# Kernel optimization log

Measured on AMD Instinct MI355X. Metric: run time of the kernel, lower is better.

## Reference

```python
import jax, jax.numpy as jnp
from jax import lax
import numpy as np

B = 64          # batch
HW = 28         # image height/width (hardcoded in module)
LATENT = 256    # latent_size
LABEL = 10      # label_size
FEAT = 64 * HW * HW  # 50176, encoder/decoder fc feature dim


def _conv(x, w, pad):
    # x: [N,C,H,W], w: [O,I,kH,kW]
    return lax.conv_general_dilated(
        x, w, (1, 1), ((pad, pad), (pad, pad)),
        dimension_numbers=('NCHW', 'OIHW', 'NCHW'))


def _conv_transpose(x, w, b, pad):
    # ConvTranspose2d(stride=1, padding=pad) == conv with flipped, transposed
    # kernel and padding k-1-pad. w: [I,O,kH,kW] (torch ConvTranspose layout).
    k = w.shape[2]
    wt = jnp.flip(w, (2, 3)).transpose(1, 0, 2, 3)  # [O,I,kH,kW]
    return _conv(x, wt, k - 1 - pad) + b[None, :, None, None]


def _encoder(images, c1w, c1b, c2w, c2b, fcw, fcb):
    x = jax.nn.relu(_conv(images, c1w, 2) + c1b[None, :, None, None])
    x = jax.nn.relu(_conv(x, c2w, 2) + c2b[None, :, None, None])
    x = x.reshape(x.shape[0], FEAT)
    return jnp.tanh(x @ fcw.T + fcb)


def _decoder(z, fcw, fcb, ct2w, ct2b, ct1w, ct1b):
    x = jnp.arctanh(z)
    x = (x @ fcw.T + fcb).reshape(-1, 64, HW, HW)
    x = jax.nn.relu(_conv_transpose(x, ct2w, ct2b, 2))
    return _conv_transpose(x, ct1w, ct1b, 2)


def _hopfield_weight(patterns):
    # TrainHopfield: Hebbian outer-product sum with mean subtraction,
    # zero diagonal, normalized by number of patterns. One GEMM.
    rho = jnp.mean(patterns)
    t = patterns - rho                      # [L, latent]
    w = t.T @ t                             # [latent, latent]
    w = w - jnp.diag(jnp.diag(w))
    return w / patterns.shape[0]


def _cluster(s0, w):
    # Batched version of: iterate s = sign(w @ s) up to LATENT steps,
    # stopping per-sample when energy -s@w@s stops changing.
    def energy(s):
        return -jnp.einsum('bi,ij,bj->b', s, w, s)

    def step(carry, _):
        s, prev_e, done = carry
        new_s = jnp.sign(s @ w.T)           # w symmetric; per-sample w@s
        e = energy(new_s)
        s_next = jnp.where(done[:, None], s, new_s)
        prev_e_next = jnp.where(done, prev_e, e)
        done_next = done | (e == prev_e)
        return (s_next, prev_e_next, done_next), None

    init = (s0, energy(s0), jnp.zeros(s0.shape[0], dtype=bool))
    (s, _, _), _ = lax.scan(step, init, None, length=LATENT)
    return s


def setup_inputs() -> dict:
    key = jax.random.key(0)
    ks = jax.random.split(key, 12)
    s = 0.05
    f32 = jnp.float32
    return {
        'images': jax.random.normal(ks[0], (B, 1, HW, HW), f32),
        'enc_c1_w': jax.random.normal(ks[1], (32, 1, 5, 5), f32) * s,
        'enc_c1_b': jnp.zeros((32,), f32),
        'enc_c2_w': jax.random.normal(ks[2], (64, 32, 5, 5), f32) * s,
        'enc_c2_b': jnp.zeros((64,), f32),
        'enc_fc_w': jax.random.normal(ks[3], (LATENT, FEAT), f32) * 0.005,
        'enc_fc_b': jnp.zeros((LATENT,), f32),
        'dec_fc_w': jax.random.normal(ks[4], (FEAT, LATENT), f32) * s,
        'dec_fc_b': jnp.zeros((FEAT,), f32),
        'dec_ct2_w': jax.random.normal(ks[5], (64, 32, 5, 5), f32) * s,
        'dec_ct2_b': jnp.zeros((32,), f32),
        'dec_ct1_w': jax.random.normal(ks[6], (32, 1, 5, 5), f32) * s,
        'dec_ct1_b': jnp.zeros((1,), f32),
        'sm_w': jax.random.normal(ks[7], (LABEL, LATENT), f32) * s,
        'sm_b': jnp.zeros((LABEL,), f32),
        'label_latent': jnp.tanh(jax.random.normal(ks[8], (LABEL, LATENT), f32)),
    }


def reference(images, enc_c1_w, enc_c1_b, enc_c2_w, enc_c2_b, enc_fc_w,
              enc_fc_b, dec_fc_w, dec_fc_b, dec_ct2_w, dec_ct2_b, dec_ct1_w,
              dec_ct1_b, sm_w, sm_b, label_latent):
    z = _encoder(images, enc_c1_w, enc_c1_b, enc_c2_w, enc_c2_b,
                 enc_fc_w, enc_fc_b)                       # [B, latent]
    w = _hopfield_weight(jnp.sign(label_latent))           # [latent, latent]
    s0 = lax.stop_gradient(jnp.sign(z))                    # detached copy
    clustered = _cluster(s0, w)                            # [B, latent]
    cluster_probs = jax.nn.softmax(clustered @ label_latent.T, axis=1)
    class_probs = jax.nn.softmax(z @ sm_w.T + sm_b, axis=1)
    recon = _decoder(z, dec_fc_w, dec_fc_b, dec_ct2_w, dec_ct2_b,
                     dec_ct1_w, dec_ct1_b)                 # [B,1,28,28]
    return (cluster_probs, class_probs, recon)
```

## Files before the change

kernel.cpp:

```cpp
#include <hip/hip_runtime.h>
#include <hip/hip_bf16.h>
#include <math.h>

#define BATCH 64
#define HW 28
#define PIX 784
#define LATENT 256
#define LABEL 10
#define FEAT 50176
#define KS 7
#define KCH 7168
#define TSTR 36

typedef __attribute__((ext_vector_type(8))) short bf16x8;
typedef __attribute__((ext_vector_type(4))) float f32x4;

__device__ __forceinline__ float sgnf(float v) {
    return (v > 0.f) ? 1.f : ((v < 0.f) ? -1.f : 0.f);
}

__device__ __forceinline__ short f2bf(float f) {
    union { float f; unsigned u; } v; v.f = f;
    unsigned r = v.u + 0x7FFF + ((v.u >> 16) & 1);
    return (short)(r >> 16);
}
__device__ __forceinline__ float bf2f(short s) {
    union { unsigned u; float f; } v; v.u = ((unsigned)(unsigned short)s) << 16;
    return v.f;
}

template<int G, int FLIP>
__global__ __launch_bounds__(256) void conv5_k(const float* __restrict__ in,
                        const float* __restrict__ w,
                        const float* __restrict__ bias, float* __restrict__ out,
                        int IC, int OC, int relu) {
    int b = blockIdx.x, oc0 = blockIdx.y * G;
    __shared__ float plp[2][32 * TSTR];
    int tid = threadIdx.x;

    for (int t = tid; t < 2 * 32 * TSTR; t += 256) ((float*)plp)[t] = 0.f;

    bool actS = tid < 196;
    int ys = tid / 7, qs = tid % 7;

    int q = tid & 7, yy = tid >> 3;
    bool actC = (q < 7) && (yy < 28);
    int x0 = q * 4;

    float acc[G][4];
    #pragma unroll
    for (int g = 0; g < G; ++g)
        #pragma unroll
        for (int xi = 0; xi < 4; ++xi) acc[g][xi] = 0.f;

    __syncthreads();
    if (actS) {
        float4 v = *(const float4*)&in[((size_t)(b * IC + 0)) * PIX + tid * 4];
        *(float2*)&plp[0][(ys + 2) * TSTR + 4 * qs + 2] = make_float2(v.x, v.y);
        *(float2*)&plp[0][(ys + 2) * TSTR + 4 * qs + 4] = make_float2(v.z, v.w);
    }
    __syncthreads();

    for (int ic = 0; ic < IC; ++ic) {
        float4 vn;
        bool more = (ic + 1) < IC;
        if (more && actS)
            vn = *(const float4*)&in[((size_t)(b * IC + ic + 1)) * PIX + tid * 4];

        const float* tile = plp[ic & 1];
        if (actC) {
            #pragma unroll
            for (int dy = 0; dy < 5; ++dy) {
                float4 ra = *(const float4*)&tile[(yy + dy) * TSTR + x0];
                float4 rb = *(const float4*)&tile[(yy + dy) * TSTR + x0 + 4];
                float rw[8] = {ra.x, ra.y, ra.z, ra.w, rb.x, rb.y, rb.z, rb.w};
                #pragma unroll
                for (int g = 0; g < G; ++g) {
                    #pragma unroll
                    for (int dx = 0; dx < 5; ++dx) {
                        float wv = FLIP
                            ? w[((size_t)ic * OC + (oc0 + g)) * 25 + (4 - dy) * 5 + (4 - dx)]
                            : w[((size_t)(oc0 + g) * IC + ic) * 25 + dy * 5 + dx];
                        #pragma unroll
                        for (int xi = 0; xi < 4; ++xi)
                            acc[g][xi] += rw[xi + dx] * wv;
                    }
                }
            }
        }
        if (more && actS) {
            float* nt = plp[(ic + 1) & 1];
            *(float2*)&nt[(ys + 2) * TSTR + 4 * qs + 2] = make_float2(vn.x, vn.y);
            *(float2*)&nt[(ys + 2) * TSTR + 4 * qs + 4] = make_float2(vn.z, vn.w);
        }
        __syncthreads();
    }

    if (actC) {
        #pragma unroll
        for (int g = 0; g < G; ++g) {
            float bv = bias[oc0 + g];
            float4 o;
            o.x = acc[g][0] + bv;
            o.y = acc[g][1] + bv;
            o.z = acc[g][2] + bv;
            o.w = acc[g][3] + bv;
            if (relu) {
                o.x = fmaxf(o.x, 0.f); o.y = fmaxf(o.y, 0.f);
                o.z = fmaxf(o.z, 0.f); o.w = fmaxf(o.w, 0.f);
            }
            *(float4*)&out[((size_t)(b * OC + (oc0 + g))) * PIX + yy * HW + x0] = o;
        }
    }
}

__global__ __launch_bounds__(64) void c2_mfma_k(const short* __restrict__ xh,
                        const short* __restrict__ xm, const short* __restrict__ xl,
                        const short* __restrict__ wb,
                        const float* __restrict__ bias, float* __restrict__ out) {
    int b = blockIdx.x;
    int t0 = blockIdx.y * 4;
    int lane = threadIdx.x;
    int prow = lane & 15, kgrp = lane >> 4;

    f32x4 acc[4][4];
    #pragma unroll
    for (int pt = 0; pt < 4; ++pt)
        #pragma unroll
        for (int nt = 0; nt < 4; ++nt) acc[pt][nt] = (f32x4){0.f, 0.f, 0.f, 0.f};

    int py[4], px[4];
    bool ptv[4];
    #pragma unroll
    for (int pt = 0; pt < 4; ++pt) {
        int p = (t0 + pt) * 16 + prow;
        ptv[pt] = (t0 + pt) < 49;
        py[pt] = p / 28; px[pt] = p % 28;
    }

    for (int tap = 0; tap < 25; ++tap) {
        int dy = tap / 5 - 2, dx = tap % 5 - 2;
        const short* wt = wb + (size_t)tap * 2048;
        bf16x8 B0[4], B1[4], B2[4];
        #pragma unroll
        for (int nt = 0; nt < 4; ++nt) {
            int off = (nt * 16 + prow) * 32 + kgrp * 8;
            B0[nt] = *(const bf16x8*)&wt[off];
            B1[nt] = *(const bf16x8*)&wt[51200 + off];
            B2[nt] = *(const bf16x8*)&wt[102400 + off];
        }
        #pragma unroll
        for (int pt = 0; pt < 4; ++pt) {
            int ysrc = py[pt] + dy, xsrc = px[pt] + dx;
            bool valid = ptv[pt] && (ysrc >= 0) && (ysrc < 28) && (xsrc >= 0) && (xsrc < 28);
            bf16x8 ah = {0,0,0,0,0,0,0,0}, am = {0,0,0,0,0,0,0,0}, al = {0,0,0,0,0,0,0,0};
            if (valid) {
                size_t o = ((size_t)b * PIX + ysrc * 28 + xsrc) * 32 + kgrp * 8;
                ah = *(const bf16x8*)&xh[o];
                am = *(const bf16x8*)&xm[o];
                al = *(const bf16x8*)&xl[o];
            }
            #pragma unroll
            for (int nt = 0; nt < 4; ++nt) {
                acc[pt][nt] = __builtin_amdgcn_mfma_f32_16x16x32_bf16(ah, B0[nt], acc[pt][nt], 0, 0, 0);
                acc[pt][nt] = __builtin_amdgcn_mfma_f32_16x16x32_bf16(ah, B1[nt], acc[pt][nt], 0, 0, 0);
                acc[pt][nt] = __builtin_amdgcn_mfma_f32_16x16x32_bf16(am, B0[nt], acc[pt][nt], 0, 0, 0);
                acc[pt][nt] = __builtin_amdgcn_mfma_f32_16x16x32_bf16(ah, B2[nt], acc[pt][nt], 0, 0, 0);
                acc[pt][nt] = __builtin_amdgcn_mfma_f32_16x16x32_bf16(am, B1[nt], acc[pt][nt], 0, 0, 0);
                acc[pt][nt] = __builtin_amdgcn_mfma_f32_16x16x32_bf16(al, B0[nt], acc[pt][nt], 0, 0, 0);
            }
        }
    }

    __shared__ float ot[64][17];
    float bv = bias[lane];
    for (int pt = 0; pt < 4; ++pt) {
        if (!ptv[pt]) continue;
        #pragma unroll
        for (int nt = 0; nt < 4; ++nt)
            #pragma unroll
            for (int r = 0; r < 4; ++r)
                ot[nt * 16 + prow][kgrp * 4 + r] = acc[pt][nt][r];
        float* op = &out[((size_t)(b * 64 + lane)) * PIX + (t0 + pt) * 16];
        #pragma unroll
        for (int i = 0; i < 4; ++i) {
            float4 o;
            o.x = fmaxf(ot[lane][i * 4 + 0] + bv, 0.f);
            o.y = fmaxf(ot[lane][i * 4 + 1] + bv, 0.f);
            o.z = fmaxf(ot[lane][i * 4 + 2] + bv, 0.f);
            o.w = fmaxf(ot[lane][i * 4 + 3] + bv, 0.f);
            *(float4*)&op[i * 4] = o;
        }
    }
}

__global__ void xsplit3_k(const float* __restrict__ x, short* __restrict__ xh,
                          short* __restrict__ xm, short* __restrict__ xl) {
    __shared__ float lds[32][17];
    int b = blockIdx.x, pbase = blockIdx.y * 16;
    int t = threadIdx.x;
    if (t < 128) {
        int ic = t >> 2, pj = (t & 3) * 4;
        float4 v = *(const float4*)&x[((size_t)(b * 32 + ic)) * PIX + pbase + pj];
        lds[ic][pj + 0] = v.x; lds[ic][pj + 1] = v.y;
        lds[ic][pj + 2] = v.z; lds[ic][pj + 3] = v.w;
    }
    __syncthreads();
    int p = t >> 4, ic2 = (t & 15) * 2;
    size_t o = ((size_t)b * PIX + pbase + p) * 32 + ic2;
    short2 h, m, l;
    {
        float v = lds[ic2][p];
        short s0 = f2bf(v); float r = v - bf2f(s0);
        short s1 = f2bf(r); float r2 = r - bf2f(s1);
        h.x = s0; m.x = s1; l.x = f2bf(r2);
    }
    {
        float v = lds[ic2 + 1][p];
        short s0 = f2bf(v); float r = v - bf2f(s0);
        short s1 = f2bf(r); float r2 = r - bf2f(s1);
        h.y = s0; m.y = s1; l.y = f2bf(r2);
    }
    *(short2*)&xh[o] = h;
    *(short2*)&xm[o] = m;
    *(short2*)&xl[o] = l;
}

__global__ void wprep3_k(const float* __restrict__ w, short* __restrict__ wb) {
    int j = blockIdx.x * 256 + threadIdx.x;
    if (j < 51200) {
        int ic = j & 31;
        int oc = (j >> 5) & 63;
        int tap = j >> 11;
        float v = w[((size_t)oc * 32 + ic) * 25 + tap];
        short s0 = f2bf(v); float r = v - bf2f(s0);
        short s1 = f2bf(r); float r2 = r - bf2f(s1);
        wb[j] = s0;
        wb[51200 + j] = s1;
        wb[102400 + j] = f2bf(r2);
    }
}

__global__ __launch_bounds__(64) void ct2_mfma_k(const short* __restrict__ xb,
                        const short* __restrict__ wb,
                        const float* __restrict__ bias, float* __restrict__ out) {
    int b = blockIdx.x;
    int pbase = blockIdx.y * 16;
    int lane = threadIdx.x;
    int prow = lane & 15;
    int kgrp = lane >> 4;
    int p = pbase + prow;
    int py = p / 28, px = p % 28;

    f32x4 acc0 = {0.f, 0.f, 0.f, 0.f};
    f32x4 acc1 = {0.f, 0.f, 0.f, 0.f};

    for (int tap = 0; tap < 25; ++tap) {
        int dy = tap / 5 - 2, dx = tap % 5 - 2;
        int ysrc = py + dy, xsrc = px + dx;
        bool valid = (ysrc >= 0) && (ysrc < 28) && (xsrc >= 0) && (xsrc < 28);
        int ps = ysrc * 28 + xsrc;

        bf16x8 a0 = {0,0,0,0,0,0,0,0}, a1 = {0,0,0,0,0,0,0,0};
        if (valid) {
            const bf16x8* ap = (const bf16x8*)&xb[((size_t)b * PIX + ps) * 64 + kgrp * 8];
            a0 = ap[0];
            a1 = ap[4];
        }
        const short* wt = &wb[(size_t)tap * 32 * 64];
        int oc_l = lane & 15;
        bf16x8 b00 = *(const bf16x8*)&wt[oc_l * 64 + kgrp * 8];
        bf16x8 b01 = *(const bf16x8*)&wt[oc_l * 64 + 32 + kgrp * 8];
        bf16x8 b10 = *(const bf16x8*)&wt[(16 + oc_l) * 64 + kgrp * 8];
        bf16x8 b11 = *(const bf16x8*)&wt[(16 + oc_l) * 64 + 32 + kgrp * 8];

        acc0 = __builtin_amdgcn_mfma_f32_16x16x32_bf16(a0, b00, acc0, 0, 0, 0);
        acc0 = __builtin_amdgcn_mfma_f32_16x16x32_bf16(a1, b01, acc0, 0, 0, 0);
        acc1 = __builtin_amdgcn_mfma_f32_16x16x32_bf16(a0, b10, acc1, 0, 0, 0);
        acc1 = __builtin_amdgcn_mfma_f32_16x16x32_bf16(a1, b11, acc1, 0, 0, 0);
    }

    __shared__ float ot[32][16];
    int drow = (lane >> 4) * 4;
    #pragma unroll
    for (int r = 0; r < 4; ++r) {
        ot[lane & 15][drow + r]        = acc0[r];
        ot[16 + (lane & 15)][drow + r] = acc1[r];
    }
    __syncthreads();
    int oc = lane >> 1, ph = (lane & 1) * 8;
    float bv = bias[oc];
    float4 o0, o1;
    o0.x = fmaxf(ot[oc][ph + 0] + bv, 0.f);
    o0.y = fmaxf(ot[oc][ph + 1] + bv, 0.f);
    o0.z = fmaxf(ot[oc][ph + 2] + bv, 0.f);
    o0.w = fmaxf(ot[oc][ph + 3] + bv, 0.f);
    o1.x = fmaxf(ot[oc][ph + 4] + bv, 0.f);
    o1.y = fmaxf(ot[oc][ph + 5] + bv, 0.f);
    o1.z = fmaxf(ot[oc][ph + 6] + bv, 0.f);
    o1.w = fmaxf(ot[oc][ph + 7] + bv, 0.f);
    float* op = &out[((size_t)(b * 32 + oc)) * PIX + pbase + ph];
    *(float4*)&op[0] = o0;
    *(float4*)&op[4] = o1;
}

__global__ void wprep_k(const float* __restrict__ w, short* __restrict__ wb) {
    int j = blockIdx.x * 256 + threadIdx.x;
    if (j < 25 * 32 * 64) {
        int ic = j & 63;
        int oc = (j >> 6) & 31;
        int tap = j >> 11;
        int dyi = tap / 5, dxi = tap % 5;
        wb[j] = f2bf(w[((size_t)ic * 32 + oc) * 25 + (4 - dyi) * 5 + (4 - dxi)]);
    }
}

__global__ void xpose_k(const float* __restrict__ x, short* __restrict__ xb) {
    __shared__ short lds[64][16];
    int b = blockIdx.x, pbase = blockIdx.y * 16;
    int t = threadIdx.x;
    {
        int ic = t >> 2, pj = (t & 3) * 4;
        float4 v = *(const float4*)&x[((size_t)(b * 64 + ic)) * PIX + pbase + pj];
        lds[ic][pj + 0] = f2bf(v.x);
        lds[ic][pj + 1] = f2bf(v.y);
        lds[ic][pj + 2] = f2bf(v.z);
        lds[ic][pj + 3] = f2bf(v.w);
    }
    __syncthreads();
    {
        int p = t >> 4, icq = (t & 15) * 4;
        short4 s;
        s.x = lds[icq + 0][p];
        s.y = lds[icq + 1][p];
        s.z = lds[icq + 2][p];
        s.w = lds[icq + 3][p];
        *(short4*)&xb[((size_t)b * PIX + pbase + p) * 64 + icq] = s;
    }
}

__global__ void enc_fc_part_k(const float* __restrict__ x, const float* __restrict__ w,
                              float* __restrict__ part) {
    int n0 = blockIdx.x * 4;
    int ks = blockIdx.y;
    int kl = threadIdx.x & 31;
    int mi = threadIdx.x >> 5;

    float acc[8][4];
    #pragma unroll
    for (int mg = 0; mg < 8; ++mg)
        #pragma unroll
        for (int nt = 0; nt < 4; ++nt) acc[mg][nt] = 0.f;

    int kend = (ks + 1) * KCH;
    for (int kk = ks * KCH + kl * 4; kk < kend; kk += 128) {
        float4 xv[8];
        #pragma unroll
        for (int mg = 0; mg < 8; ++mg)
            xv[mg] = *(const float4*)&x[(size_t)(mg * 8 + mi) * FEAT + kk];
        #pragma unroll
        for (int nt = 0; nt < 4; ++nt) {
            float4 wv = *(const float4*)&w[(size_t)(n0 + nt) * FEAT + kk];
            #pragma unroll
            for (int mg = 0; mg < 8; ++mg) {
                acc[mg][nt] += xv[mg].x * wv.x + xv[mg].y * wv.y
                             + xv[mg].z * wv.z + xv[mg].w * wv.w;
            }
        }
    }

    #pragma unroll
    for (int mg = 0; mg < 8; ++mg) {
        #pragma unroll
        for (int nt = 0; nt < 4; ++nt) {
            float v = acc[mg][nt];
            v += __shfl_xor(v, 16, 64);
            v += __shfl_xor(v, 8, 64);
            v += __shfl_xor(v, 4, 64);
            v += __shfl_xor(v, 2, 64);
            v += __shfl_xor(v, 1, 64);
            if (kl == 0)
                part[(ks * BATCH + (mg * 8 + mi)) * LATENT + (n0 + nt)] = v;
        }
    }
}

__global__ void enc_fc_fin_k(const float* __restrict__ part, const float* __restrict__ bias,
                             float* __restrict__ z, float* __restrict__ xsaT) {
    int m = blockIdx.x;
    int n = threadIdx.x;
    int idx = m * 256 + n;
    float a = bias[n];
    for (int ksi = 0; ksi < KS; ++ksi) a += part[ksi * BATCH * LATENT + idx];
    float zv = tanhf(a);
    z[idx] = zv;
    xsaT[n * BATCH + m] = atanhf(zv);
}

__global__ void hop_rho_k(const float* __restrict__ ll, float* __restrict__ rho_out) {
    float p = 0.f;
    for (int t = threadIdx.x; t < LABEL * LATENT; t += 256) p += sgnf(ll[t]);
    __shared__ float red[8];
    for (int o = 32; o; o >>= 1) p += __shfl_down(p, o, 64);
    if ((threadIdx.x & 63) == 0) red[threadIdx.x >> 6] = p;
    __syncthreads();
    if (threadIdx.x == 0)
        rho_out[0] = (red[0] + red[1] + red[2] + red[3]) / (float)(LABEL * LATENT);
}

__global__ void hop_w_k(const float* __restrict__ ll, const float* __restrict__ rho_p,
                        float* __restrict__ wout) {
    int i = blockIdx.x, j = threadIdx.x;
    float rho = rho_p[0];
    float acc = 0.f;
    #pragma unroll
    for (int l = 0; l < LABEL; ++l) {
        float a = sgnf(ll[l * LATENT + i]) - rho;
        float b = sgnf(ll[l * LATENT + j]) - rho;
        acc += a * b;
    }
    wout[i * LATENT + j] = (i == j) ? 0.f : acc / 10.f;
}

__global__ __launch_bounds__(1024) void cluster_k(const float* __restrict__ z,
                          const float* __restrict__ w,
                          const float* __restrict__ ll, float* __restrict__ out) {
    int b = blockIdx.x;
    int t = threadIdx.x;
    int i = t & 255;
    int q = t >> 8;
    int lane = t & 63;
    int wvid = t >> 6;

    __shared__ float s_sh[LATENT];
    __shared__ float part[1024];
    __shared__ float red[4];
    __shared__ float cflag[4];
    __shared__ int ctl_sh;
    __shared__ float logit[LABEL];

    float wreg[64];
    #pragma unroll
    for (int jj = 0; jj < 64; ++jj)
        wreg[jj] = w[(q * 64 + jj) * LATENT + i];

    float s_cur = 0.f, s_old = 2.f, v = 0.f;
    float e_prev = 0.f;
    if (q == 0) {
        s_cur = sgnf(z[b * LATENT + i]);
        s_sh[i] = s_cur;
    }
    __syncthreads();

    {
        float p0 = 0.f, p1 = 0.f;
        #pragma unroll
        for (int jj = 0; jj < 64; jj += 2) {
            p0 += wreg[jj]     * s_sh[q * 64 + jj];
            p1 += wreg[jj + 1] * s_sh[q * 64 + jj + 1];
        }
        part[t] = p0 + p1;
    }
    __syncthreads();
    if (q == 0) {
        v = part[i] + part[i + 256] + part[i + 512] + part[i + 768];
        float p = s_cur * v;
        #pragma unroll
        for (int o = 32; o; o >>= 1) p += __shfl_down(p, o, 64);
        if (lane == 0) red[wvid] = p;
    }
    __syncthreads();
    if (t == 0) e_prev = -(red[0] + red[1] + red[2] + red[3]);

    for (int it = 0; it < LATENT; ++it) {
        if (q == 0) {
            float ns = sgnf(v);
            unsigned long long m = __ballot(ns == s_old);
            if (lane == 0) cflag[wvid] = (m == ~0ull) ? 1.f : 0.f;
            s_sh[i] = ns;
            s_old = s_cur;
            s_cur = ns;
        }
        __syncthreads();
        {
            float p0 = 0.f, p1 = 0.f;
            #pragma unroll
            for (int jj = 0; jj < 64; jj += 2) {
                p0 += wreg[jj]     * s_sh[q * 64 + jj];
                p1 += wreg[jj + 1] * s_sh[q * 64 + jj + 1];
            }
            part[t] = p0 + p1;
        }
        __syncthreads();
        if (q == 0) {
            v = part[i] + part[i + 256] + part[i + 512] + part[i + 768];
            float p = s_cur * v;
            #pragma unroll
            for (int o = 32; o; o >>= 1) p += __shfl_down(p, o, 64);
            if (lane == 0) red[wvid] = p;
        }
        __syncthreads();
        if (t == 0) {
            float e = -(red[0] + red[1] + red[2] + red[3]);
            int c = 0;
            if (e == e_prev) c = 1;
            else if (it >= 1 && cflag[0] != 0.f && cflag[1] != 0.f &&
                     cflag[2] != 0.f && cflag[3] != 0.f)
                c = (((LATENT - 1 - it) & 1) == 0) ? 2 : 3;
            else e_prev = e;
            ctl_sh = c;
        }
        __syncthreads();
        int c = ctl_sh;
        if (c != 0) {
            if (c == 3 && q == 0) s_sh[i] = s_old;
            break;
        }
    }
    __syncthreads();

    if (wvid < LABEL) {
        float p = 0.f;
        #pragma unroll
        for (int r = 0; r < 4; ++r)
            p += s_sh[r * 64 + lane] * ll[wvid * LATENT + r * 64 + lane];
        #pragma unroll
        for (int o = 32; o; o >>= 1) p += __shfl_down(p, o, 64);
        if (lane == 0) logit[wvid] = p;
    }
    __syncthreads();
    if (t == 0) {
        float mx = logit[0];
        for (int c = 1; c < LABEL; ++c) mx = fmaxf(mx, logit[c]);
        float ex[LABEL];
        float s = 0.f;
        for (int c = 0; c < LABEL; ++c) { ex[c] = expf(logit[c] - mx); s += ex[c]; }
        for (int c = 0; c < LABEL; ++c) out[b * LABEL + c] = ex[c] / s;
    }
}

__device__ __forceinline__ float block_sum256(float p, float* red) {
    __syncthreads();
    for (int o = 32; o; o >>= 1) p += __shfl_down(p, o, 64);
    if ((threadIdx.x & 63) == 0) red[threadIdx.x >> 6] = p;
    __syncthreads();
    return red[0] + red[1] + red[2] + red[3];
}

__global__ void class_k(const float* __restrict__ z, const float* __restrict__ smw,
                        const float* __restrict__ smb, float* __restrict__ out) {
    int b = blockIdx.x;
    int i = threadIdx.x;
    __shared__ float red[8];
    __shared__ float logit[LABEL];
    float zi = z[b * LATENT + i];
    for (int c = 0; c < LABEL; ++c) {
        float p = zi * smw[c * LATENT + i];
        float t = block_sum256(p, red);
        if (i == 0) logit[c] = t + smb[c];
    }
    __syncthreads();
    if (i == 0) {
        float mx = logit[0];
        for (int c = 1; c < LABEL; ++c) mx = fmaxf(mx, logit[c]);
        float ex[LABEL];
        float s = 0.f;
        for (int c = 0; c < LABEL; ++c) { ex[c] = expf(logit[c] - mx); s += ex[c]; }
        for (int c = 0; c < LABEL; ++c) out[b * LABEL + c] = ex[c] / s;
    }
}

__global__ __launch_bounds__(256) void dec_fc_k(const float* __restrict__ xsa,
                         const float* __restrict__ w,
                         const float* __restrict__ bias, float* __restrict__ y) {
    __shared__ float xs[128 * BATCH];
    __shared__ float wt[64 * 128];
    int tid = threadIdx.x;
    int lane = tid & 63;
    int wv = tid >> 6;
    int n0 = blockIdx.x * 64;

    float acc[16];
    #pragma unroll
    for (int nt = 0; nt < 16; ++nt) acc[nt] = 0.f;

    float4 xr[8], wr[8];
    #pragma unroll
    for (int i = 0; i < 8; ++i) {
        int j = i * 1024 + tid * 4;
        xr[i] = *(const float4*)&xsa[j];
        int row = j >> 7, col = j & 127;
        wr[i] = *(const float4*)&w[(size_t)(n0 + row) * LATENT + col];
    }
    #pragma unroll
    for (int i = 0; i < 8; ++i) {
        int j = i * 1024 + tid * 4;
        *(float4*)&xs[j] = xr[i];
        *(float4*)&wt[j] = wr[i];
    }
    __syncthreads();

    #pragma unroll
    for (int i = 0; i < 8; ++i) {
        int j = i * 1024 + tid * 4;
        xr[i] = *(const float4*)&xsa[8192 + j];
        int row = j >> 7, col = j & 127;
        wr[i] = *(const float4*)&w[(size_t)(n0 + row) * LATENT + 128 + col];
    }

    for (int kq = 0; kq < 32; ++kq) {
        int k0 = kq * 4;
        float xv0 = xs[(k0 + 0) * BATCH + lane];
        float xv1 = xs[(k0 + 1) * BATCH + lane];
        float xv2 = xs[(k0 + 2) * BATCH + lane];
        float xv3 = xs[(k0 + 3) * BATCH + lane];
        #pragma unroll
        for (int nt = 0; nt < 16; ++nt) {
            float4 wv4 = *(const float4*)&wt[(wv * 16 + nt) * 128 + k0];
            acc[nt] += xv0 * wv4.x + xv1 * wv4.y + xv2 * wv4.z + xv3 * wv4.w;
        }
    }
    __syncthreads();

    #pragma unroll
    for (int i = 0; i < 8; ++i) {
        int j = i * 1024 + tid * 4;
        *(float4*)&xs[j] = xr[i];
        *(float4*)&wt[j] = wr[i];
    }
    __syncthreads();

    for (int kq = 0; kq < 32; ++kq) {
        int k0 = kq * 4;
        float xv0 = xs[(k0 + 0) * BATCH + lane];
        float xv1 = xs[(k0 + 1) * BATCH + lane];
        float xv2 = xs[(k0 + 2) * BATCH + lane];
        float xv3 = xs[(k0 + 3) * BATCH + lane];
        #pragma unroll
        for (int nt = 0; nt < 16; ++nt) {
            float4 wv4 = *(const float4*)&wt[(wv * 16 + nt) * 128 + k0];
            acc[nt] += xv0 * wv4.x + xv1 * wv4.y + xv2 * wv4.z + xv3 * wv4.w;
        }
    }

    int nbase = n0 + wv * 16;
    #pragma unroll
    for (int nq = 0; nq < 4; ++nq) {
        float4 o;
        o.x = acc[nq * 4 + 0] + bias[nbase + nq * 4 + 0];
        o.y = acc[nq * 4 + 1] + bias[nbase + nq * 4 + 1];
        o.z = acc[nq * 4 + 2] + bias[nbase + nq * 4 + 2];
        o.w = acc[nq * 4 + 3] + bias[nbase + nq * 4 + 3];
        *(float4*)&y[(size_t)lane * FEAT + nbase + nq * 4] = o;
    }
}

extern "C" void kernel_launch(void* const* d_in, const int* in_sizes, int n_in,
                              void* d_out, int out_size, void* d_ws, size_t ws_size,
                              hipStream_t stream) {
    const float* images   = (const float*)d_in[0];
    const float* c1w      = (const float*)d_in[1];
    const float* c1b      = (const float*)d_in[2];
    const float* c2w      = (const float*)d_in[3];
    const float* c2b      = (const float*)d_in[4];
    const float* efw      = (const float*)d_in[5];
    const float* efb      = (const float*)d_in[6];
    const float* dfw      = (const float*)d_in[7];
    const float* dfb      = (const float*)d_in[8];
    const float* ct2w     = (const float*)d_in[9];
    const float* ct2b     = (const float*)d_in[10];
    const float* ct1w     = (const float*)d_in[11];
    const float* ct1b     = (const float*)d_in[12];
    const float* smw      = (const float*)d_in[13];
    const float* smb      = (const float*)d_in[14];
    const float* ll       = (const float*)d_in[15];

    float* out = (float*)d_out;
    float* ws  = (float*)d_ws;

    float* big0 = ws;
    float* big1 = ws + 3211264;
    float* part = ws + 3211264 + 1605632;
    float* z    = part + KS * BATCH * LATENT;
    float* whop = z + BATCH * LATENT;
    float* rho  = whop + LATENT * LATENT;
    float* xsa  = rho + 4;
    short* xbf  = (short*)(xsa + 16384);
    short* wbf  = (short*)(xsa + 16384 + 1605632);
    short* xh3  = xbf;
    short* xm3  = xbf + 1605632;
    short* xl3  = (short*)(xsa + 16384 + 1605632 + 25600);
    short* wb3  = xl3 + 1605632;

    conv5_k<4,0><<<dim3(BATCH, 8), 256, 0, stream>>>(images, c1w, c1b, big1, 1, 32, 1);
    wprep3_k<<<200, 256, 0, stream>>>(c2w, wb3);
    xsplit3_k<<<dim3(BATCH, 49), 256, 0, stream>>>(big1, xh3, xm3, xl3);
    c2_mfma_k<<<dim3(BATCH, 13), 64, 0, stream>>>(xh3, xm3, xl3, wb3, c2b, big0);
    enc_fc_part_k<<<dim3(64, KS), 256, 0, stream>>>(big0, efw, part);
    enc_fc_fin_k<<<BATCH, 256, 0, stream>>>(part, efb, z, xsa);

    hop_rho_k<<<1, 256, 0, stream>>>(ll, rho);
    hop_w_k<<<LATENT, 256, 0, stream>>>(ll, rho, whop);
    cluster_k<<<BATCH, 1024, 0, stream>>>(z, whop, ll, out);
    class_k<<<BATCH, 256, 0, stream>>>(z, smw, smb, out + 640);

    wprep_k<<<200, 256, 0, stream>>>(ct2w, wbf);
    dec_fc_k<<<FEAT / 64, 256, 0, stream>>>(xsa, dfw, dfb, big0);
    xpose_k<<<dim3(BATCH, 49), 256, 0, stream>>>(big0, xbf);
    ct2_mfma_k<<<dim3(BATCH, 49), 64, 0, stream>>>(xbf, wbf, ct2b, big1);
    conv5_k<1,1><<<dim3(BATCH, 1), 256, 0, stream>>>(big1, ct1w, ct1b, out + 1280, 32, 1, 0);
}
```

Baseline: 337.4 us.

## Move decoder FC to bf16 MFMA with split activations and bf16 output

Replaces the fp32 LDS-tiled decoder FC GEMM with a bf16 MFMA kernel. Activations are split into high and residual bf16 parts, while weights are converted to bf16 on the fly. The kernel writes a bf16 intermediate, so the transpose kernel reads shorts instead of floats, halving that traffic. Separately, the encoder FC split-K factor rises from 7 to 28 for more parallelism. Rounding the weights to bf16 loses some accuracy, and the larger split-K adds partial-sum traffic.

```diff
diff --git a/kernel.cpp b/kernel.cpp
--- a/kernel.cpp
+++ b/kernel.cpp
@@ -8,8 +8,8 @@
 #define LATENT 256
 #define LABEL 10
 #define FEAT 50176
-#define KS 7
-#define KCH 7168
+#define KS 28
+#define KCH 1792
 #define TSTR 36
 
 typedef __attribute__((ext_vector_type(8))) short bf16x8;
@@ -315,17 +315,17 @@
     }
 }
 
-__global__ void xpose_k(const float* __restrict__ x, short* __restrict__ xb) {
+__global__ void xpose16_k(const short* __restrict__ y16, short* __restrict__ xb) {
     __shared__ short lds[64][16];
     int b = blockIdx.x, pbase = blockIdx.y * 16;
     int t = threadIdx.x;
     {
         int ic = t >> 2, pj = (t & 3) * 4;
-        float4 v = *(const float4*)&x[((size_t)(b * 64 + ic)) * PIX + pbase + pj];
-        lds[ic][pj + 0] = f2bf(v.x);
-        lds[ic][pj + 1] = f2bf(v.y);
-        lds[ic][pj + 2] = f2bf(v.z);
-        lds[ic][pj + 3] = f2bf(v.w);
+        short4 v = *(const short4*)&y16[((size_t)(b * 64 + ic)) * PIX + pbase + pj];
+        lds[ic][pj + 0] = v.x;
+        lds[ic][pj + 1] = v.y;
+        lds[ic][pj + 2] = v.z;
+        lds[ic][pj + 3] = v.w;
     }
     __syncthreads();
     {
@@ -386,7 +386,8 @@
 }
 
 __global__ void enc_fc_fin_k(const float* __restrict__ part, const float* __restrict__ bias,
-                             float* __restrict__ z, float* __restrict__ xsaT) {
+                             float* __restrict__ z, short* __restrict__ xah,
+                             short* __restrict__ xam) {
     int m = blockIdx.x;
     int n = threadIdx.x;
     int idx = m * 256 + n;
@@ -394,7 +395,10 @@
     for (int ksi = 0; ksi < KS; ++ksi) a += part[ksi * BATCH * LATENT + idx];
     float zv = tanhf(a);
     z[idx] = zv;
-    xsaT[n * BATCH + m] = atanhf(zv);
+    float xv = atanhf(zv);
+    short h = f2bf(xv);
+    xah[idx] = h;
+    xam[idx] = f2bf(xv - bf2f(h));
 }
 
 __global__ void hop_rho_k(const float* __restrict__ ll, float* __restrict__ rho_out) {
@@ -570,88 +574,52 @@
     }
 }
 
-__global__ __launch_bounds__(256) void dec_fc_k(const float* __restrict__ xsa,
+__global__ __launch_bounds__(256) void dec_fc_mfma_k(const short* __restrict__ xah,
+                         const short* __restrict__ xam,
                          const float* __restrict__ w,
-                         const float* __restrict__ bias, float* __restrict__ y) {
-    __shared__ float xs[128 * BATCH];
-    __shared__ float wt[64 * 128];
+                         const float* __restrict__ bias, short* __restrict__ y16) {
     int tid = threadIdx.x;
-    int lane = tid & 63;
-    int wv = tid >> 6;
+    int lane = tid & 63, wv = tid >> 6;
+    int prow = lane & 15, kgrp = lane >> 4;
     int n0 = blockIdx.x * 64;
-
-    float acc[16];
-    #pragma unroll
-    for (int nt = 0; nt < 16; ++nt) acc[nt] = 0.f;
-
-    float4 xr[8], wr[8];
-    #pragma unroll
-    for (int i = 0; i < 8; ++i) {
-        int j = i * 1024 + tid * 4;
-        xr[i] = *(const float4*)&xsa[j];
-        int row = j >> 7, col = j & 127;
-        wr[i] = *(const float4*)&w[(size_t)(n0 + row) * LATENT + col];
-    }
-    #pragma unroll
-    for (int i = 0; i < 8; ++i) {
-        int j = i * 1024 + tid * 4;
-        *(float4*)&xs[j] = xr[i];
-        *(float4*)&wt[j] = wr[i];
-    }
-    __syncthreads();
-
-    #pragma unroll
-    for (int i = 0; i < 8; ++i) {
-        int j = i * 1024 + tid * 4;
-        xr[i] = *(const float4*)&xsa[8192 + j];
-        int row = j >> 7, col = j & 127;
-        wr[i] = *(const float4*)&w[(size_t)(n0 + row) * LATENT + 128 + col];
-    }
-
-    for (int kq = 0; kq < 32; ++kq) {
-        int k0 = kq * 4;
-        float xv0 = xs[(k0 + 0) * BATCH + lane];
-        float xv1 = xs[(k0 + 1) * BATCH + lane];
-        float xv2 = xs[(k0 + 2) * BATCH + lane];
-        float xv3 = xs[(k0 + 3) * BATCH + lane];
-        #pragma unroll
-        for (int nt = 0; nt < 16; ++nt) {
-            float4 wv4 = *(const float4*)&wt[(wv * 16 + nt) * 128 + k0];
-            acc[nt] += xv0 * wv4.x + xv1 * wv4.y + xv2 * wv4.z + xv3 * wv4.w;
-        }
-    }
-    __syncthreads();
-
-    #pragma unroll
-    for (int i = 0; i < 8; ++i) {
-        int j = i * 1024 + tid * 4;
-        *(float4*)&xs[j] = xr[i];
-        *(float4*)&wt[j] = wr[i];
-    }
-    __syncthreads();
-
-    for (int kq = 0; kq < 32; ++kq) {
-        int k0 = kq * 4;
-        float xv0 = xs[(k0 + 0) * BATCH + lane];
-        float xv1 = xs[(k0 + 1) * BATCH + lane];
-        float xv2 = xs[(k0 + 2) * BATCH + lane];
-        float xv3 = xs[(k0 + 3) * BATCH + lane];
-        #pragma unroll
-        for (int nt = 0; nt < 16; ++nt) {
-            float4 wv4 = *(const float4*)&wt[(wv * 16 + nt) * 128 + k0];
-            acc[nt] += xv0 * wv4.x + xv1 * wv4.y + xv2 * wv4.z + xv3 * wv4.w;
-        }
-    }
-
-    int nbase = n0 + wv * 16;
-    #pragma unroll
-    for (int nq = 0; nq < 4; ++nq) {
-        float4 o;
-        o.x = acc[nq * 4 + 0] + bias[nbase + nq * 4 + 0];
-        o.y = acc[nq * 4 + 1] + bias[nbase + nq * 4 + 1];
-        o.z = acc[nq * 4 + 2] + bias[nbase + nq * 4 + 2];
-        o.w = acc[nq * 4 + 3] + bias[nbase + nq * 4 + 3];
-        *(float4*)&y[(size_t)lane * FEAT + nbase + nq * 4] = o;
+    int nb = n0 + wv * 16;
+
+    f32x4 acc[4];
+    #pragma unroll
+    for (int mi = 0; mi < 4; ++mi) acc[mi] = (f32x4){0.f, 0.f, 0.f, 0.f};
+
+    for (int kc = 0; kc < 8; ++kc) {
+        int kof = kc * 32 + kgrp * 8;
+        const float* wp = &w[(size_t)(nb + prow) * LATENT + kof];
+        float4 w0 = *(const float4*)&wp[0];
+        float4 w1 = *(const float4*)&wp[4];
+        bf16x8 bf;
+        bf[0] = f2bf(w0.x); bf[1] = f2bf(w0.y); bf[2] = f2bf(w0.z); bf[3] = f2bf(w0.w);
+        bf[4] = f2bf(w1.x); bf[5] = f2bf(w1.y); bf[6] = f2bf(w1.z); bf[7] = f2bf(w1.w);
+        #pragma unroll
+        for (int mi = 0; mi < 4; ++mi) {
+            bf16x8 ah = *(const bf16x8*)&xah[(mi * 16 + prow) * LATENT + kof];
+            bf16x8 am = *(const bf16x8*)&xam[(mi * 16 + prow) * LATENT + kof];
+            acc[mi] = __builtin_amdgcn_mfma_f32_16x16x32_bf16(ah, bf, acc[mi], 0, 0, 0);
+            acc[mi] = __builtin_amdgcn_mfma_f32_16x16x32_bf16(am, bf, acc[mi], 0, 0, 0);
+        }
+    }
+
+    __shared__ short ot[64 * 72];
+    float bv = bias[nb + prow];
+    #pragma unroll
+    for (int mi = 0; mi < 4; ++mi)
+        #pragma unroll
+        for (int r = 0; r < 4; ++r) {
+            int m = mi * 16 + kgrp * 4 + r;
+            ot[m * 72 + wv * 16 + prow] = f2bf(acc[mi][r] + bv);
+        }
+    __syncthreads();
+    int m = tid >> 2, q = tid & 3;
+    #pragma unroll
+    for (int i = 0; i < 2; ++i) {
+        *(int4*)&y16[(size_t)m * FEAT + n0 + i * 32 + q * 8] =
+            *(int4*)&ot[m * 72 + i * 32 + q * 8];
     }
 }
 
@@ -685,19 +653,22 @@
     float* whop = z + BATCH * LATENT;
     float* rho  = whop + LATENT * LATENT;
     float* xsa  = rho + 4;
+    short* xah  = (short*)xsa;
+    short* xam  = xah + 16384;
     short* xbf  = (short*)(xsa + 16384);
     short* wbf  = (short*)(xsa + 16384 + 1605632);
     short* xh3  = xbf;
     short* xm3  = xbf + 1605632;
     short* xl3  = (short*)(xsa + 16384 + 1605632 + 25600);
     short* wb3  = xl3 + 1605632;
+    short* y16  = (short*)big0;
 
     conv5_k<4,0><<<dim3(BATCH, 8), 256, 0, stream>>>(images, c1w, c1b, big1, 1, 32, 1);
     wprep3_k<<<200, 256, 0, stream>>>(c2w, wb3);
     xsplit3_k<<<dim3(BATCH, 49), 256, 0, stream>>>(big1, xh3, xm3, xl3);
     c2_mfma_k<<<dim3(BATCH, 13), 64, 0, stream>>>(xh3, xm3, xl3, wb3, c2b, big0);
     enc_fc_part_k<<<dim3(64, KS), 256, 0, stream>>>(big0, efw, part);
-    enc_fc_fin_k<<<BATCH, 256, 0, stream>>>(part, efb, z, xsa);
+    enc_fc_fin_k<<<BATCH, 256, 0, stream>>>(part, efb, z, xah, xam);
 
     hop_rho_k<<<1, 256, 0, stream>>>(ll, rho);
     hop_w_k<<<LATENT, 256, 0, stream>>>(ll, rho, whop);
@@ -705,8 +676,8 @@
     class_k<<<BATCH, 256, 0, stream>>>(z, smw, smb, out + 640);
 
     wprep_k<<<200, 256, 0, stream>>>(ct2w, wbf);
-    dec_fc_k<<<FEAT / 64, 256, 0, stream>>>(xsa, dfw, dfb, big0);
-    xpose_k<<<dim3(BATCH, 49), 256, 0, stream>>>(big0, xbf);
+    dec_fc_mfma_k<<<FEAT / 64, 256, 0, stream>>>(xah, xam, dfw, dfb, y16);
+    xpose16_k<<<dim3(BATCH, 49), 256, 0, stream>>>(y16, xbf);
     ct2_mfma_k<<<dim3(BATCH, 49), 64, 0, stream>>>(xbf, wbf, ct2b, big1);
     conv5_k<1,1><<<dim3(BATCH, 1), 256, 0, stream>>>(big1, ct1w, ct1b, out + 1280, 32, 1, 0);
 }
```

After: 295.9 us. 12.3% less time.
